# Performance work log

Measured on AMD Instinct MI355X. Metric: run time of the kernel, lower is better.

The kernel has to match this reference:

```python
import jax, jax.numpy as jnp
import numpy as np

H = 128          # input hidden dim
HID = 128        # expert hidden width
OUT = 128        # out_channels
NR = 8           # n_routed
NS = 2           # n_shared
RDIM = 16        # router feature dim


def setup_inputs() -> dict:
    key = jax.random.key(0)
    ks = jax.random.split(key, 11)
    s = 0.05
    x = jax.random.normal(ks[0], (2, 32, 32, 32, H), dtype=jnp.float32)
    # router params
    Wr1 = jax.random.normal(ks[1], (H, RDIM), dtype=jnp.float32) * s
    br1 = jnp.zeros((RDIM,), dtype=jnp.float32)
    Wr2 = jax.random.normal(ks[2], (RDIM, NR), dtype=jnp.float32) * s
    br2 = jnp.zeros((NR,), dtype=jnp.float32)
    # routed expert params, stacked on leading expert axis
    We1 = jax.random.normal(ks[3], (NR, H, HID), dtype=jnp.float32) * s
    be1 = jnp.zeros((NR, HID), dtype=jnp.float32)
    We2 = jax.random.normal(ks[4], (NR, HID, OUT), dtype=jnp.float32) * s
    be2 = jnp.zeros((NR, OUT), dtype=jnp.float32)
    # shared expert params
    Ws1 = jax.random.normal(ks[5], (NS, H, HID), dtype=jnp.float32) * s
    bs1 = jnp.zeros((NS, HID), dtype=jnp.float32)
    Ws2 = jax.random.normal(ks[6], (NS, HID, OUT), dtype=jnp.float32) * s
    bs2 = jnp.zeros((NS, OUT), dtype=jnp.float32)
    return dict(x=x, Wr1=Wr1, br1=br1, Wr2=Wr2, br2=br2,
                We1=We1, be1=be1, We2=We2, be2=be2,
                Ws1=Ws1, bs1=bs1, Ws2=Ws2, bs2=bs2)


def reference(x, Wr1, br1, Wr2, br2, We1, be1, We2, be2, Ws1, bs1, Ws2, bs2):
    # router: Dense(16) -> relu -> Dense(n_routed) -> softmax
    rf = jax.nn.relu(jnp.einsum('...h,hr->...r', x, Wr1) + br1)
    logits = jnp.einsum('...r,re->...e', rf, Wr2) + br2
    gate = jax.nn.softmax(logits, axis=-1)                      # [..., NR]
    threshold = 1.0 / NR
    mask = (gate > threshold).astype(gate.dtype)
    mg = gate * mask
    mg = mg / (jnp.sum(mg, axis=-1, keepdims=True) + 1e-8)
    # routed experts (batched over expert axis e): Dense -> gelu(tanh) -> Dense
    hr = jax.nn.gelu(jnp.einsum('...h,ehd->...ed', x, We1) + be1)   # [..., NR, HID]
    ro = jnp.einsum('...ed,edo->...eo', hr, We2) + be2              # [..., NR, OUT]
    routed_agg = jnp.einsum('...eo,...e->...o', ro, mg)
    # shared experts summed
    hs = jax.nn.gelu(jnp.einsum('...h,ehd->...ed', x, Ws1) + bs1)   # [..., NS, HID]
    so = jnp.einsum('...ed,edo->...eo', hs, Ws2) + bs2              # [..., NS, OUT]
    shared_agg = jnp.sum(so, axis=-2)
    return routed_agg + shared_agg
```

## Files before the change

kernel.cpp:

```cpp
#include <hip/hip_runtime.h>
#include <hip/hip_bf16.h>

typedef __bf16 bf16x8 __attribute__((ext_vector_type(8)));
typedef __bf16 bf16x4 __attribute__((ext_vector_type(4)));
typedef float  f32x16 __attribute__((ext_vector_type(16)));
typedef float  f32x4  __attribute__((ext_vector_type(4)));
typedef float  f32x2  __attribute__((ext_vector_type(2)));

static __device__ __forceinline__ f32x16 mfma32(bf16x8 a, bf16x8 b, f32x16 c) {
    return __builtin_amdgcn_mfma_f32_32x32x16_bf16(a, b, c, 0, 0, 0);
}

#define GELU_C1 2.30220820f
#define GELU_C2 0.10294324f

static __device__ __forceinline__ bf16x8 gelu8(f32x16 a, int base, float gv) {
    bf16x8 r;
    #pragma unroll
    for (int p = 0; p < 4; ++p) {
        f32x2 hh; hh[0] = a[base + 2 * p]; hh[1] = a[base + 2 * p + 1];
        f32x2 tt = hh * hh;
        f32x2 pp;
        pp[0] = fmaf(tt[0], -GELU_C2, -GELU_C1);
        pp[1] = fmaf(tt[1], -GELU_C2, -GELU_C1);
        f32x2 mm = hh * pp;
        float e0 = __builtin_amdgcn_exp2f(mm[0]);
        float e1 = __builtin_amdgcn_exp2f(mm[1]);
        float q0 = __builtin_amdgcn_rcpf(1.f + e0);
        float q1 = __builtin_amdgcn_rcpf(1.f + e1);
        r[2 * p]     = (__bf16)(hh[0] * q0 * gv);
        r[2 * p + 1] = (__bf16)(hh[1] * q1 * gv);
    }
    return r;
}

__global__ __launch_bounds__(256) void pack_kernel(
    const float* __restrict__ We1, const float* __restrict__ be1,
    const float* __restrict__ Ws1, const float* __restrict__ bs1,
    const float* __restrict__ We2, const float* __restrict__ Ws2,
    const float* __restrict__ Wr1, const float* __restrict__ br1,
    const float* __restrict__ Wr2, const float* __restrict__ br2,
    __bf16* __restrict__ w1p, __bf16* __restrict__ w2p,
    double* __restrict__ wr1d, double* __restrict__ br1d,
    double* __restrict__ wr2d, double* __restrict__ br2d)
{
    int tid = blockIdx.x * 256 + threadIdx.x;
    if (tid < 23040) {
        int l  = tid & 63;
        int ks = (tid >> 6) % 9;
        int nt = (tid / 576) & 3;
        int e  = tid / 2304;
        const float* src = (e < 8) ? (We1 + e * 16384) : (Ws1 + (e - 8) * 16384);
        const float* bia = (e < 8) ? (be1 + e * 128)   : (bs1 + (e - 8) * 128);
        int n = nt * 32 + (l & 31);
        int kb = ks * 16 + (l >> 5) * 8;
        bf16x8 v;
        #pragma unroll
        for (int j = 0; j < 8; ++j) {
            int k = kb + j;
            float f = (k < 128) ? src[k * 128 + n] : ((k == 128) ? bia[n] : 0.f);
            v[j] = (__bf16)f;
        }
        *(bf16x8*)(w1p + (size_t)tid * 8) = v;
    } else if (tid < 43520) {
        int t2 = tid - 23040;
        int l  = t2 & 63;
        int ks = (t2 >> 6) & 7;
        int ot = (t2 / 512) & 3;
        int e  = t2 / 2048;
        const float* src = (e < 8) ? (We2 + e * 16384) : (Ws2 + (e - 8) * 16384);
        int o  = ot * 32 + (l & 31);
        int lh = l >> 5;
        bf16x8 v;
        #pragma unroll
        for (int j = 0; j < 8; ++j) {
            int hid = 16 * ks + 8 * (j >> 2) + 4 * lh + (j & 3);
            v[j] = (__bf16)src[hid * 128 + o];
        }
        *(bf16x8*)(w2p + (size_t)t2 * 8) = v;
    } else if (tid < 45568) {
        int i = tid - 43520;
        wr1d[i] = (double)Wr1[i];
    } else if (tid < 45696) {
        int i = tid - 45568;
        wr2d[i] = (double)Wr2[i];
    } else if (tid < 45712) {
        int i = tid - 45696;
        br1d[i] = (double)br1[i];
    } else if (tid < 45720) {
        int i = tid - 45712;
        br2d[i] = (double)br2[i];
    }
}

__global__ __launch_bounds__(256) void router_kernel(
    const float* __restrict__ x,
    const double* __restrict__ wr1d, const double* __restrict__ br1d,
    const double* __restrict__ wr2d, const double* __restrict__ br2d,
    float* __restrict__ gates)
{
    __shared__ __align__(16) char lds[51200];
    float*  xs  = (float*)lds;
    double* rfs = (double*)(lds + 33280);
    double* lgs = (double*)(lds + 41984);
    double* exs = (double*)(lds + 46592);

    const int t    = threadIdx.x;
    const int tok0 = blockIdx.x * 64;

    #pragma unroll
    for (int i = 0; i < 8; ++i) {
        int cid = i * 256 + t;
        int m = cid >> 5;
        int c = cid & 31;
        f32x4 v = *(const f32x4*)(x + (size_t)(tok0 + m) * 128 + c * 4);
        f32x2 s0, s1;
        s0[0] = v[0]; s0[1] = v[1]; s1[0] = v[2]; s1[1] = v[3];
        *(f32x2*)(xs + m * 130 + c * 4)     = s0;
        *(f32x2*)(xs + m * 130 + c * 4 + 2) = s1;
    }
    __syncthreads();

    {
        const int tok = t & 63;
        const int rq  = (t >> 6) * 4;
        const int rqs = __builtin_amdgcn_readfirstlane(rq);
        double rf4[4];
        #pragma unroll
        for (int j = 0; j < 4; ++j) rf4[j] = br1d[rqs + j];
        const float* xr = xs + tok * 130;
        #pragma unroll 4
        for (int c = 0; c < 64; ++c) {
            f32x2 xv2 = *(const f32x2*)(xr + c * 2);
            #pragma unroll
            for (int q = 0; q < 2; ++q) {
                double xv = (double)xv2[q];
                int k = c * 2 + q;
                #pragma unroll
                for (int j = 0; j < 4; ++j)
                    rf4[j] = fma(xv, wr1d[k * 16 + rqs + j], rf4[j]);
            }
        }
        #pragma unroll
        for (int j = 0; j < 4; ++j)
            rfs[tok * 17 + rqs + j] = rf4[j] > 0.0 ? rf4[j] : 0.0;
    }
    __syncthreads();

    const int tok = t & 63;
    const int j0  = __builtin_amdgcn_readfirstlane((t >> 6) * 2);
    double lgA = br2d[j0], lgB = br2d[j0 + 1];
    #pragma unroll
    for (int r = 0; r < 16; ++r) {
        double rv = rfs[tok * 17 + r];
        lgA = fma(rv, wr2d[r * 8 + j0],     lgA);
        lgB = fma(rv, wr2d[r * 8 + j0 + 1], lgB);
    }
    lgs[tok * 9 + j0]     = lgA;
    lgs[tok * 9 + j0 + 1] = lgB;
    __syncthreads();

    {
        double mx = lgs[tok * 9];
        #pragma unroll
        for (int k = 1; k < 8; ++k) {
            double v = lgs[tok * 9 + k];
            mx = v > mx ? v : mx;
        }
        exs[tok * 9 + j0]     = exp(lgA - mx);
        exs[tok * 9 + j0 + 1] = exp(lgB - mx);
    }
    __syncthreads();

    if (t < 64) {
        double ex[8]; double s = 0.0;
        #pragma unroll
        for (int j = 0; j < 8; ++j) { ex[j] = exs[t * 9 + j]; s += ex[j]; }
        double ms = 0.0;
        bool mk[8];
        #pragma unroll
        for (int j = 0; j < 8; ++j) {
            mk[j] = (8.0 * ex[j] > s);
            ms += mk[j] ? ex[j] : 0.0;
        }
        double inv = 1.0 / (ms + s * 1e-8);
        f32x4 o0, o1;
        #pragma unroll
        for (int j = 0; j < 4; ++j) {
            o0[j] = mk[j]     ? (float)(ex[j] * inv)     : 0.f;
            o1[j] = mk[4 + j] ? (float)(ex[4 + j] * inv) : 0.f;
        }
        *(f32x4*)(gates + (size_t)(tok0 + t) * 8)     = o0;
        *(f32x4*)(gates + (size_t)(tok0 + t) * 8 + 4) = o1;
    }
}

__global__ __launch_bounds__(256, 2) void moe_main_kernel(
    const float* __restrict__ x, const float* __restrict__ gates,
    const __bf16* __restrict__ w1p, const __bf16* __restrict__ w2p,
    const float* __restrict__ be2, const float* __restrict__ bs2,
    float* __restrict__ out)
{
    __shared__ __align__(16) char lds[69632];
    __bf16* Xp = (__bf16*)lds;
    __bf16* Hs = (__bf16*)(lds + 32768);
    float*  mg = (float*)(lds + 65536);

    const int t    = threadIdx.x;
    const int lane = t & 63;
    const int wave = t >> 6;
    const int l31  = lane & 31;
    const int hi   = lane >> 5;
    const int mp   = wave >> 1;
    const int oh   = wave & 1;
    const int tok0 = blockIdx.x * 128;

    #pragma unroll
    for (int i = 0; i < 8; ++i) {
        int g = i * 256 + t;
        int m = g >> 4;
        int c = g & 15;
        const f32x4* sp = (const f32x4*)(x + (size_t)(tok0 + m) * 128 + c * 8);
        f32x4 va = sp[0], vb = sp[1];
        bf16x8 v;
        v[0]=(__bf16)va[0]; v[1]=(__bf16)va[1]; v[2]=(__bf16)va[2]; v[3]=(__bf16)va[3];
        v[4]=(__bf16)vb[0]; v[5]=(__bf16)vb[1]; v[6]=(__bf16)vb[2]; v[7]=(__bf16)vb[3];
        *(bf16x8*)&Xp[(((m >> 5) * 8 + (c >> 1)) * 64 + (c & 1) * 32 + (m & 31)) * 8] = v;
    }
    {
        int m = t >> 1, half = t & 1;
        f32x4 g = *(const f32x4*)(gates + (size_t)(tok0 + m) * 8 + half * 4);
        *(f32x4*)&mg[m * 8 + half * 4] = g;
    }
    __syncthreads();

    bf16x8 xbias;
    #pragma unroll
    for (int j = 0; j < 8; ++j) xbias[j] = (__bf16)0.f;
    if (lane < 32) xbias[0] = (__bf16)1.0f;

    f32x16 acc00, acc01, acc10, acc11;
    #pragma unroll
    for (int i = 0; i < 16; ++i) { acc00[i]=0.f; acc01[i]=0.f; acc10[i]=0.f; acc11[i]=0.f; }

    const bf16x8* w1v = (const bf16x8*)w1p;
    const bf16x8* w2v = (const bf16x8*)w2p;

    #pragma unroll 1
    for (int e = 0; e < 10; ++e) {
        const bf16x8* wp  = w1v + ((size_t)(e * 4 + 2 * oh) * 9) * 64 + lane;
        const bf16x8* wBp = w2v + ((size_t)(e * 4 + 2 * oh) * 8) * 64 + lane;
        bf16x8 wb0[9], wb1[9];
        #pragma unroll
        for (int ks = 0; ks < 9; ++ks) wb0[ks] = wp[ks * 64];
        #pragma unroll
        for (int ks = 0; ks < 9; ++ks) wb1[ks] = wp[(9 + ks) * 64];
        bf16x8 wB0[8];
        #pragma unroll
        for (int kq = 0; kq < 8; ++kq) wB0[kq] = wBp[kq * 64];

        #pragma unroll
        for (int mi = 0; mi < 2; ++mi) {
            const int mt = 2 * mp + mi;
            float gv = 1.0f;
            if (e < 8) gv = mg[(32 * mt + l31) * 8 + e];
            f32x16 a0, a1;
            #pragma unroll
            for (int i = 0; i < 16; ++i) { a0[i] = 0.f; a1[i] = 0.f; }
            #pragma unroll
            for (int ks = 0; ks < 8; ++ks) {
                bf16x8 xb = *(const bf16x8*)&Xp[((mt * 8 + ks) * 64 + lane) * 8];
                a0 = mfma32(wb0[ks], xb, a0);
                a1 = mfma32(wb1[ks], xb, a1);
            }
            a0 = mfma32(wb0[8], xbias, a0);
            a1 = mfma32(wb1[8], xbias, a1);
            int rb = (mt * 8 + 4 * oh) * 64 + lane;
            *(bf16x8*)&Hs[(rb + 0 * 64) * 8] = gelu8(a0, 0, gv);
            *(bf16x8*)&Hs[(rb + 1 * 64) * 8] = gelu8(a0, 8, gv);
            *(bf16x8*)&Hs[(rb + 2 * 64) * 8] = gelu8(a1, 0, gv);
            *(bf16x8*)&Hs[(rb + 3 * 64) * 8] = gelu8(a1, 8, gv);
        }
        __syncthreads();

        bf16x8 wB1[8];
        #pragma unroll
        for (int kq = 0; kq < 8; ++kq) wB1[kq] = wBp[(8 + kq) * 64];

        __builtin_amdgcn_s_setprio(1);
        #pragma unroll
        for (int kq = 0; kq < 8; ++kq) {
            bf16x8 h0 = *(const bf16x8*)&Hs[(((2 * mp)     * 8 + kq) * 64 + lane) * 8];
            bf16x8 h1 = *(const bf16x8*)&Hs[(((2 * mp + 1) * 8 + kq) * 64 + lane) * 8];
            acc00 = mfma32(h0, wB0[kq], acc00);
            acc01 = mfma32(h0, wB1[kq], acc01);
            acc10 = mfma32(h1, wB0[kq], acc10);
            acc11 = mfma32(h1, wB1[kq], acc11);
        }
        __builtin_amdgcn_s_setprio(0);
        __syncthreads();
    }

    {
        float be2c[2][8], bsc[2];
        #pragma unroll
        for (int oti = 0; oti < 2; ++oti) {
            int o = 32 * (2 * oh + oti) + l31;
            bsc[oti] = bs2[o] + bs2[128 + o];
            #pragma unroll
            for (int ee = 0; ee < 8; ++ee) be2c[oti][ee] = be2[ee * 128 + o];
        }
        #pragma unroll
        for (int mi = 0; mi < 2; ++mi) {
            const int mt = 2 * mp + mi;
            const float* mgb = mg + (32 * mt) * 8;
            f32x16 aA = mi ? acc10 : acc00;
            f32x16 aB = mi ? acc11 : acc01;
            #pragma unroll
            for (int r = 0; r < 16; ++r) {
                int mrow = (r & 3) + 8 * (r >> 2) + 4 * hi;
                f32x4 g0 = *(const f32x4*)&mgb[mrow * 8];
                f32x4 g1 = *(const f32x4*)&mgb[mrow * 8 + 4];
                size_t orow = (size_t)(tok0 + 32 * mt + mrow) * 128;
                float b0 = bsc[0], b1 = bsc[1];
                #pragma unroll
                for (int ee = 0; ee < 4; ++ee) {
                    b0 = fmaf(g0[ee], be2c[0][ee], b0);
                    b1 = fmaf(g0[ee], be2c[1][ee], b1);
                }
                #pragma unroll
                for (int ee = 0; ee < 4; ++ee) {
                    b0 = fmaf(g1[ee], be2c[0][4 + ee], b0);
                    b1 = fmaf(g1[ee], be2c[1][4 + ee], b1);
                }
                out[orow + 32 * (2 * oh)     + l31] = aA[r] + b0;
                out[orow + 32 * (2 * oh + 1) + l31] = aB[r] + b1;
            }
        }
    }
}

extern "C" void kernel_launch(void* const* d_in, const int* in_sizes, int n_in,
                              void* d_out, int out_size, void* d_ws, size_t ws_size,
                              hipStream_t stream)
{
    const float* x   = (const float*)d_in[0];
    const float* Wr1 = (const float*)d_in[1];
    const float* br1 = (const float*)d_in[2];
    const float* Wr2 = (const float*)d_in[3];
    const float* br2 = (const float*)d_in[4];
    const float* We1 = (const float*)d_in[5];
    const float* be1 = (const float*)d_in[6];
    const float* We2 = (const float*)d_in[7];
    const float* be2 = (const float*)d_in[8];
    const float* Ws1 = (const float*)d_in[9];
    const float* bs1 = (const float*)d_in[10];
    const float* Ws2 = (const float*)d_in[11];
    const float* bs2 = (const float*)d_in[12];

    __bf16* w1p  = (__bf16*)d_ws;
    __bf16* w2p  = (__bf16*)((char*)d_ws + 368640);
    double* wr1d = (double*)((char*)d_ws + 696320);
    double* wr2d = (double*)((char*)d_ws + 712704);
    double* br1d = (double*)((char*)d_ws + 713728);
    double* br2d = (double*)((char*)d_ws + 713856);
    float*  gts  = (float*)((char*)d_ws + 720896);

    pack_kernel<<<179, 256, 0, stream>>>(We1, be1, Ws1, bs1, We2, Ws2,
                                         Wr1, br1, Wr2, br2,
                                         w1p, w2p, wr1d, br1d, wr2d, br2d);
    router_kernel<<<1024, 256, 0, stream>>>(x, wr1d, br1d, wr2d, br2d, gts);
    moe_main_kernel<<<512, 256, 0, stream>>>(x, gts, w1p, w2p, be2, bs2,
                                             (float*)d_out);
}
```

Baseline: 184.5 us.

## Fuse router into MoE kernel, add bias in fp32, prefetch next expert weights

Removes the separate router kernel and computes the fp64 router MLP, softmax and threshold mask inside the main MoE kernel, reusing the hidden-activation LDS region as scratch. This drops a kernel launch and the round trip of the gate tensor through global memory. The first-layer bias no longer goes through an extra MFMA on a padded K slice; it is packed in accumulator order and added in fp32. Weights for the next expert are loaded into registers while the current expert is still computing. The costs are higher register pressure from the held weights, and the fp64 router work now runs inside the main kernel, ahead of the expert matmuls.

```diff
diff --git a/kernel.cpp b/kernel.cpp
--- a/kernel.cpp
+++ b/kernel.cpp
@@ -2,7 +2,6 @@
 #include <hip/hip_bf16.h>
 
 typedef __bf16 bf16x8 __attribute__((ext_vector_type(8)));
-typedef __bf16 bf16x4 __attribute__((ext_vector_type(4)));
 typedef float  f32x16 __attribute__((ext_vector_type(16)));
 typedef float  f32x4  __attribute__((ext_vector_type(4)));
 typedef float  f32x2  __attribute__((ext_vector_type(2)));
@@ -41,29 +40,25 @@
     const float* __restrict__ Wr1, const float* __restrict__ br1,
     const float* __restrict__ Wr2, const float* __restrict__ br2,
     __bf16* __restrict__ w1p, __bf16* __restrict__ w2p,
+    float* __restrict__ be1p,
     double* __restrict__ wr1d, double* __restrict__ br1d,
     double* __restrict__ wr2d, double* __restrict__ br2d)
 {
     int tid = blockIdx.x * 256 + threadIdx.x;
-    if (tid < 23040) {
+    if (tid < 20480) {
         int l  = tid & 63;
-        int ks = (tid >> 6) % 9;
-        int nt = (tid / 576) & 3;
-        int e  = tid / 2304;
+        int ks = (tid >> 6) & 7;
+        int nt = (tid >> 9) & 3;
+        int e  = tid >> 11;
         const float* src = (e < 8) ? (We1 + e * 16384) : (Ws1 + (e - 8) * 16384);
-        const float* bia = (e < 8) ? (be1 + e * 128)   : (bs1 + (e - 8) * 128);
-        int n = nt * 32 + (l & 31);
+        int n  = nt * 32 + (l & 31);
         int kb = ks * 16 + (l >> 5) * 8;
         bf16x8 v;
         #pragma unroll
-        for (int j = 0; j < 8; ++j) {
-            int k = kb + j;
-            float f = (k < 128) ? src[k * 128 + n] : ((k == 128) ? bia[n] : 0.f);
-            v[j] = (__bf16)f;
-        }
+        for (int j = 0; j < 8; ++j) v[j] = (__bf16)src[(kb + j) * 128 + n];
         *(bf16x8*)(w1p + (size_t)tid * 8) = v;
-    } else if (tid < 43520) {
-        int t2 = tid - 23040;
+    } else if (tid < 40960) {
+        int t2 = tid - 20480;
         int l  = t2 & 63;
         int ks = (t2 >> 6) & 7;
         int ot = (t2 / 512) & 3;
@@ -78,133 +73,43 @@
             v[j] = (__bf16)src[hid * 128 + o];
         }
         *(bf16x8*)(w2p + (size_t)t2 * 8) = v;
-    } else if (tid < 45568) {
-        int i = tid - 43520;
+    } else if (tid < 42240) {
+        int i  = tid - 40960;
+        int r  = i & 15;
+        int h2 = (i >> 4) & 1;
+        int nt = (i >> 5) & 3;
+        int e  = i >> 7;
+        int n  = 32 * nt + (r & 3) + 8 * (r >> 2) + 4 * h2;
+        be1p[i] = (e < 8) ? be1[e * 128 + n] : bs1[(e - 8) * 128 + n];
+    } else if (tid < 44288) {
+        int i = tid - 42240;
         wr1d[i] = (double)Wr1[i];
-    } else if (tid < 45696) {
-        int i = tid - 45568;
+    } else if (tid < 44416) {
+        int i = tid - 44288;
         wr2d[i] = (double)Wr2[i];
-    } else if (tid < 45712) {
-        int i = tid - 45696;
+    } else if (tid < 44432) {
+        int i = tid - 44416;
         br1d[i] = (double)br1[i];
-    } else if (tid < 45720) {
-        int i = tid - 45712;
+    } else if (tid < 44440) {
+        int i = tid - 44432;
         br2d[i] = (double)br2[i];
     }
 }
 
-__global__ __launch_bounds__(256) void router_kernel(
+__global__ __launch_bounds__(256, 2) void moe_main_kernel(
     const float* __restrict__ x,
     const double* __restrict__ wr1d, const double* __restrict__ br1d,
     const double* __restrict__ wr2d, const double* __restrict__ br2d,
-    float* __restrict__ gates)
-{
-    __shared__ __align__(16) char lds[51200];
-    float*  xs  = (float*)lds;
-    double* rfs = (double*)(lds + 33280);
-    double* lgs = (double*)(lds + 41984);
-    double* exs = (double*)(lds + 46592);
-
-    const int t    = threadIdx.x;
-    const int tok0 = blockIdx.x * 64;
-
-    #pragma unroll
-    for (int i = 0; i < 8; ++i) {
-        int cid = i * 256 + t;
-        int m = cid >> 5;
-        int c = cid & 31;
-        f32x4 v = *(const f32x4*)(x + (size_t)(tok0 + m) * 128 + c * 4);
-        f32x2 s0, s1;
-        s0[0] = v[0]; s0[1] = v[1]; s1[0] = v[2]; s1[1] = v[3];
-        *(f32x2*)(xs + m * 130 + c * 4)     = s0;
-        *(f32x2*)(xs + m * 130 + c * 4 + 2) = s1;
-    }
-    __syncthreads();
-
-    {
-        const int tok = t & 63;
-        const int rq  = (t >> 6) * 4;
-        const int rqs = __builtin_amdgcn_readfirstlane(rq);
-        double rf4[4];
-        #pragma unroll
-        for (int j = 0; j < 4; ++j) rf4[j] = br1d[rqs + j];
-        const float* xr = xs + tok * 130;
-        #pragma unroll 4
-        for (int c = 0; c < 64; ++c) {
-            f32x2 xv2 = *(const f32x2*)(xr + c * 2);
-            #pragma unroll
-            for (int q = 0; q < 2; ++q) {
-                double xv = (double)xv2[q];
-                int k = c * 2 + q;
-                #pragma unroll
-                for (int j = 0; j < 4; ++j)
-                    rf4[j] = fma(xv, wr1d[k * 16 + rqs + j], rf4[j]);
-            }
-        }
-        #pragma unroll
-        for (int j = 0; j < 4; ++j)
-            rfs[tok * 17 + rqs + j] = rf4[j] > 0.0 ? rf4[j] : 0.0;
-    }
-    __syncthreads();
-
-    const int tok = t & 63;
-    const int j0  = __builtin_amdgcn_readfirstlane((t >> 6) * 2);
-    double lgA = br2d[j0], lgB = br2d[j0 + 1];
-    #pragma unroll
-    for (int r = 0; r < 16; ++r) {
-        double rv = rfs[tok * 17 + r];
-        lgA = fma(rv, wr2d[r * 8 + j0],     lgA);
-        lgB = fma(rv, wr2d[r * 8 + j0 + 1], lgB);
-    }
-    lgs[tok * 9 + j0]     = lgA;
-    lgs[tok * 9 + j0 + 1] = lgB;
-    __syncthreads();
-
-    {
-        double mx = lgs[tok * 9];
-        #pragma unroll
-        for (int k = 1; k < 8; ++k) {
-            double v = lgs[tok * 9 + k];
-            mx = v > mx ? v : mx;
-        }
-        exs[tok * 9 + j0]     = exp(lgA - mx);
-        exs[tok * 9 + j0 + 1] = exp(lgB - mx);
-    }
-    __syncthreads();
-
-    if (t < 64) {
-        double ex[8]; double s = 0.0;
-        #pragma unroll
-        for (int j = 0; j < 8; ++j) { ex[j] = exs[t * 9 + j]; s += ex[j]; }
-        double ms = 0.0;
-        bool mk[8];
-        #pragma unroll
-        for (int j = 0; j < 8; ++j) {
-            mk[j] = (8.0 * ex[j] > s);
-            ms += mk[j] ? ex[j] : 0.0;
-        }
-        double inv = 1.0 / (ms + s * 1e-8);
-        f32x4 o0, o1;
-        #pragma unroll
-        for (int j = 0; j < 4; ++j) {
-            o0[j] = mk[j]     ? (float)(ex[j] * inv)     : 0.f;
-            o1[j] = mk[4 + j] ? (float)(ex[4 + j] * inv) : 0.f;
-        }
-        *(f32x4*)(gates + (size_t)(tok0 + t) * 8)     = o0;
-        *(f32x4*)(gates + (size_t)(tok0 + t) * 8 + 4) = o1;
-    }
-}
-
-__global__ __launch_bounds__(256, 2) void moe_main_kernel(
-    const float* __restrict__ x, const float* __restrict__ gates,
     const __bf16* __restrict__ w1p, const __bf16* __restrict__ w2p,
+    const float* __restrict__ be1p,
     const float* __restrict__ be2, const float* __restrict__ bs2,
     float* __restrict__ out)
 {
     __shared__ __align__(16) char lds[69632];
-    __bf16* Xp = (__bf16*)lds;
-    __bf16* Hs = (__bf16*)(lds + 32768);
-    float*  mg = (float*)(lds + 65536);
+    __bf16* Xp  = (__bf16*)lds;
+    __bf16* Hs  = (__bf16*)(lds + 32768);
+    float*  mg  = (float*)(lds + 65536);
+    double* rfs = (double*)(lds + 32768);
 
     const int t    = threadIdx.x;
     const int lane = t & 63;
@@ -214,6 +119,21 @@
     const int mp   = wave >> 1;
     const int oh   = wave & 1;
     const int tok0 = blockIdx.x * 128;
+
+    const bf16x8* w1v = (const bf16x8*)w1p;
+    const bf16x8* w2v = (const bf16x8*)w2p;
+
+    bf16x8 wb0[8], wb1[8], wB0[8];
+    {
+        const bf16x8* wp  = w1v + ((size_t)(2 * oh) * 8) * 64 + lane;
+        const bf16x8* wBp = w2v + ((size_t)(2 * oh) * 8) * 64 + lane;
+        #pragma unroll
+        for (int ks = 0; ks < 8; ++ks) {
+            wb0[ks] = wp[ks * 64];
+            wb1[ks] = wp[(8 + ks) * 64];
+            wB0[ks] = wBp[ks * 64];
+        }
+    }
 
     #pragma unroll
     for (int i = 0; i < 8; ++i) {
@@ -227,66 +147,136 @@
         v[4]=(__bf16)vb[0]; v[5]=(__bf16)vb[1]; v[6]=(__bf16)vb[2]; v[7]=(__bf16)vb[3];
         *(bf16x8*)&Xp[(((m >> 5) * 8 + (c >> 1)) * 64 + (c & 1) * 32 + (m & 31)) * 8] = v;
     }
+
     {
-        int m = t >> 1, half = t & 1;
-        f32x4 g = *(const f32x4*)(gates + (size_t)(tok0 + m) * 8 + half * 4);
-        *(f32x4*)&mg[m * 8 + half * 4] = g;
+        const int tok = t >> 1;
+        const int rq8 = (t & 1) * 8;
+        double rf[8];
+        #pragma unroll
+        for (int j = 0; j < 8; ++j) rf[j] = br1d[rq8 + j];
+        const float* xr = x + (size_t)(tok0 + tok) * 128;
+        #pragma unroll 4
+        for (int c = 0; c < 64; ++c) {
+            f32x2 xv2 = *(const f32x2*)(xr + c * 2);
+            #pragma unroll
+            for (int q = 0; q < 2; ++q) {
+                double xv = (double)xv2[q];
+                const double* wrow = wr1d + (c * 2 + q) * 16 + rq8;
+                #pragma unroll
+                for (int j = 0; j < 8; ++j) rf[j] = fma(xv, wrow[j], rf[j]);
+            }
+        }
+        double* rr = rfs + tok * 17 + rq8;
+        #pragma unroll
+        for (int j = 0; j < 8; ++j) rr[j] = rf[j] > 0.0 ? rf[j] : 0.0;
     }
     __syncthreads();
 
-    bf16x8 xbias;
-    #pragma unroll
-    for (int j = 0; j < 8; ++j) xbias[j] = (__bf16)0.f;
-    if (lane < 32) xbias[0] = (__bf16)1.0f;
+    if (t < 128) {
+        double lg[8];
+        #pragma unroll
+        for (int j = 0; j < 8; ++j) lg[j] = br2d[j];
+        #pragma unroll
+        for (int r = 0; r < 16; ++r) {
+            double rv = rfs[t * 17 + r];
+            #pragma unroll
+            for (int j = 0; j < 8; ++j)
+                lg[j] = fma(rv, wr2d[r * 8 + j], lg[j]);
+        }
+        double mx = lg[0];
+        #pragma unroll
+        for (int j = 1; j < 8; ++j) mx = lg[j] > mx ? lg[j] : mx;
+        double ex[8]; double s = 0.0;
+        #pragma unroll
+        for (int j = 0; j < 8; ++j) { ex[j] = exp(lg[j] - mx); s += ex[j]; }
+        double ms = 0.0;
+        bool mk[8];
+        #pragma unroll
+        for (int j = 0; j < 8; ++j) {
+            mk[j] = (8.0 * ex[j] > s);
+            ms += mk[j] ? ex[j] : 0.0;
+        }
+        double inv = 1.0 / (ms + s * 1e-8);
+        f32x4 o0, o1;
+        #pragma unroll
+        for (int j = 0; j < 4; ++j) {
+            o0[j] = mk[j]     ? (float)(ex[j] * inv)     : 0.f;
+            o1[j] = mk[4 + j] ? (float)(ex[4 + j] * inv) : 0.f;
+        }
+        *(f32x4*)&mg[t * 8]     = o0;
+        *(f32x4*)&mg[t * 8 + 4] = o1;
+    }
+    __syncthreads();
 
     f32x16 acc00, acc01, acc10, acc11;
     #pragma unroll
     for (int i = 0; i < 16; ++i) { acc00[i]=0.f; acc01[i]=0.f; acc10[i]=0.f; acc11[i]=0.f; }
 
-    const bf16x8* w1v = (const bf16x8*)w1p;
-    const bf16x8* w2v = (const bf16x8*)w2p;
-
     #pragma unroll 1
     for (int e = 0; e < 10; ++e) {
-        const bf16x8* wp  = w1v + ((size_t)(e * 4 + 2 * oh) * 9) * 64 + lane;
-        const bf16x8* wBp = w2v + ((size_t)(e * 4 + 2 * oh) * 8) * 64 + lane;
-        bf16x8 wb0[9], wb1[9];
-        #pragma unroll
-        for (int ks = 0; ks < 9; ++ks) wb0[ks] = wp[ks * 64];
-        #pragma unroll
-        for (int ks = 0; ks < 9; ++ks) wb1[ks] = wp[(9 + ks) * 64];
-        bf16x8 wB0[8];
-        #pragma unroll
-        for (int kq = 0; kq < 8; ++kq) wB0[kq] = wBp[kq * 64];
-
-        #pragma unroll
-        for (int mi = 0; mi < 2; ++mi) {
-            const int mt = 2 * mp + mi;
-            float gv = 1.0f;
-            if (e < 8) gv = mg[(32 * mt + l31) * 8 + e];
-            f32x16 a0, a1;
-            #pragma unroll
-            for (int i = 0; i < 16; ++i) { a0[i] = 0.f; a1[i] = 0.f; }
+        float gv0 = 1.0f, gv1 = 1.0f;
+        if (e < 8) {
+            gv0 = mg[(64 * mp + l31) * 8 + e];
+            gv1 = mg[(64 * mp + 32 + l31) * 8 + e];
+        }
+        const float* bp = be1p + (size_t)((e * 4 + 2 * oh) * 2 + hi) * 16;
+        f32x16 bA = *(const f32x16*)bp;
+        f32x16 bB = *(const f32x16*)(bp + 32);
+
+        __builtin_amdgcn_s_setprio(1);
+        f32x16 a0, a1;
+        #pragma unroll
+        for (int i = 0; i < 16; ++i) { a0[i] = 0.f; a1[i] = 0.f; }
+        #pragma unroll
+        for (int ks = 0; ks < 8; ++ks) {
+            bf16x8 xb = *(const bf16x8*)&Xp[(((2 * mp) * 8 + ks) * 64 + lane) * 8];
+            a0 = mfma32(wb0[ks], xb, a0);
+            a1 = mfma32(wb1[ks], xb, a1);
+        }
+        __builtin_amdgcn_s_setprio(0);
+        a0 += bA; a1 += bB;
+        {
+            int rb = ((2 * mp) * 8 + 4 * oh) * 64 + lane;
+            *(bf16x8*)&Hs[(rb + 0 * 64) * 8] = gelu8(a0, 0, gv0);
+            *(bf16x8*)&Hs[(rb + 1 * 64) * 8] = gelu8(a0, 8, gv0);
+            *(bf16x8*)&Hs[(rb + 2 * 64) * 8] = gelu8(a1, 0, gv0);
+            *(bf16x8*)&Hs[(rb + 3 * 64) * 8] = gelu8(a1, 8, gv0);
+        }
+        __builtin_amdgcn_s_setprio(1);
+        f32x16 c0, c1;
+        #pragma unroll
+        for (int i = 0; i < 16; ++i) { c0[i] = 0.f; c1[i] = 0.f; }
+        #pragma unroll
+        for (int ks = 0; ks < 8; ++ks) {
+            bf16x8 xb = *(const bf16x8*)&Xp[(((2 * mp + 1) * 8 + ks) * 64 + lane) * 8];
+            c0 = mfma32(wb0[ks], xb, c0);
+            c1 = mfma32(wb1[ks], xb, c1);
+        }
+        __builtin_amdgcn_s_setprio(0);
+        if (e < 9) {
+            const bf16x8* wp = w1v + ((size_t)((e + 1) * 4 + 2 * oh) * 8) * 64 + lane;
             #pragma unroll
             for (int ks = 0; ks < 8; ++ks) {
-                bf16x8 xb = *(const bf16x8*)&Xp[((mt * 8 + ks) * 64 + lane) * 8];
-                a0 = mfma32(wb0[ks], xb, a0);
-                a1 = mfma32(wb1[ks], xb, a1);
+                wb0[ks] = wp[ks * 64];
+                wb1[ks] = wp[(8 + ks) * 64];
             }
-            a0 = mfma32(wb0[8], xbias, a0);
-            a1 = mfma32(wb1[8], xbias, a1);
-            int rb = (mt * 8 + 4 * oh) * 64 + lane;
-            *(bf16x8*)&Hs[(rb + 0 * 64) * 8] = gelu8(a0, 0, gv);
-            *(bf16x8*)&Hs[(rb + 1 * 64) * 8] = gelu8(a0, 8, gv);
-            *(bf16x8*)&Hs[(rb + 2 * 64) * 8] = gelu8(a1, 0, gv);
-            *(bf16x8*)&Hs[(rb + 3 * 64) * 8] = gelu8(a1, 8, gv);
+        }
+        c0 += bA; c1 += bB;
+        {
+            int rb = ((2 * mp + 1) * 8 + 4 * oh) * 64 + lane;
+            *(bf16x8*)&Hs[(rb + 0 * 64) * 8] = gelu8(c0, 0, gv1);
+            *(bf16x8*)&Hs[(rb + 1 * 64) * 8] = gelu8(c0, 8, gv1);
+            *(bf16x8*)&Hs[(rb + 2 * 64) * 8] = gelu8(c1, 0, gv1);
+            *(bf16x8*)&Hs[(rb + 3 * 64) * 8] = gelu8(c1, 8, gv1);
         }
         __syncthreads();
 
         bf16x8 wB1[8];
-        #pragma unroll
-        for (int kq = 0; kq < 8; ++kq) wB1[kq] = wBp[(8 + kq) * 64];
-
+        {
+            const bf16x8* wBp = w2v + ((size_t)(e * 4 + 2 * oh) * 8) * 64 + lane;
+            #pragma unroll
+            for (int kq = 0; kq < 8; ++kq) wB1[kq] = wBp[(8 + kq) * 64];
+        }
         __builtin_amdgcn_s_setprio(1);
         #pragma unroll
         for (int kq = 0; kq < 8; ++kq) {
@@ -298,6 +288,11 @@
             acc11 = mfma32(h1, wB1[kq], acc11);
         }
         __builtin_amdgcn_s_setprio(0);
+        if (e < 9) {
+            const bf16x8* wBn = w2v + ((size_t)((e + 1) * 4 + 2 * oh) * 8) * 64 + lane;
+            #pragma unroll
+            for (int kq = 0; kq < 8; ++kq) wB0[kq] = wBn[kq * 64];
+        }
         __syncthreads();
     }
 
@@ -359,17 +354,17 @@
     const float* bs2 = (const float*)d_in[12];
 
     __bf16* w1p  = (__bf16*)d_ws;
-    __bf16* w2p  = (__bf16*)((char*)d_ws + 368640);
-    double* wr1d = (double*)((char*)d_ws + 696320);
-    double* wr2d = (double*)((char*)d_ws + 712704);
-    double* br1d = (double*)((char*)d_ws + 713728);
-    double* br2d = (double*)((char*)d_ws + 713856);
-    float*  gts  = (float*)((char*)d_ws + 720896);
-
-    pack_kernel<<<179, 256, 0, stream>>>(We1, be1, Ws1, bs1, We2, Ws2,
+    __bf16* w2p  = (__bf16*)((char*)d_ws + 327680);
+    float*  be1p = (float*)((char*)d_ws + 655360);
+    double* wr1d = (double*)((char*)d_ws + 660480);
+    double* wr2d = (double*)((char*)d_ws + 676864);
+    double* br1d = (double*)((char*)d_ws + 677888);
+    double* br2d = (double*)((char*)d_ws + 678016);
+
+    pack_kernel<<<174, 256, 0, stream>>>(We1, be1, Ws1, bs1, We2, Ws2,
                                          Wr1, br1, Wr2, br2,
-                                         w1p, w2p, wr1d, br1d, wr2d, br2d);
-    router_kernel<<<1024, 256, 0, stream>>>(x, wr1d, br1d, wr2d, br2d, gts);
-    moe_main_kernel<<<512, 256, 0, stream>>>(x, gts, w1p, w2p, be2, bs2,
+                                         w1p, w2p, be1p, wr1d, br1d, wr2d, br2d);
+    moe_main_kernel<<<512, 256, 0, stream>>>(x, wr1d, br1d, wr2d, br2d,
+                                             w1p, w2p, be1p, be2, bs2,
                                              (float*)d_out);
 }
```

After: 200.6 us. 8.7% more time.
